# Performance work log

Hardware: AMD Instinct MI355X
Metric: run time of the kernel (lower is better)

The kernel has to match this reference:

```python
import jax, jax.numpy as jnp
import numpy as np

NBITS = 16  # posit word size passed to posit_forward
ES = 1      # posit exponent-field size (standard posit16 uses es=1)


def posit_quant(x, nbits=NBITS, es=ES):
    """Round-trip float -> posit(nbits, es) -> float, vectorized.

    Emulates posit quantization: regime length determines how many fraction
    bits remain, mantissa is rounded to that precision, magnitude clamped to
    [minpos, maxpos]. Straight-through estimator keeps gradients useful.
    """
    absx = jnp.abs(x)
    sign = jnp.sign(x)
    safe = jnp.maximum(absx, 1e-30)
    scale = jnp.floor(jnp.log2(safe))                 # binary exponent
    useed_log2 = float(2 ** es)
    regime = jnp.floor(scale / useed_log2)
    rlen = jnp.where(regime >= 0, regime + 2.0, 1.0 - regime)  # regime bits
    fbits = jnp.clip(nbits - 1 - es - rlen, 0.0, 28.0)          # fraction bits left
    pw = jnp.exp2(fbits)
    m = safe * jnp.exp2(-scale)                       # mantissa in [1, 2)
    mq = 1.0 + jnp.round((m - 1.0) * pw) / pw
    maxscale = float((nbits - 2) * (2 ** es))         # maxpos = 2^((n-2)*2^es)
    mag = jnp.clip(mq * jnp.exp2(scale), jnp.exp2(-maxscale), jnp.exp2(maxscale))
    q = jnp.where(absx == 0.0, 0.0, sign * mag)
    return x + jax.lax.stop_gradient(q - x)           # straight-through


def posit_linear(x, W, b):
    # posit_forward: quantize operands, GEMM, quantize the accumulated output
    xq = posit_quant(x)
    Wq = posit_quant(W)
    bq = posit_quant(b)
    return posit_quant(xq @ Wq.T + bq)


def setup_inputs() -> dict:
    key = jax.random.key(0)
    ks = jax.random.split(key, 7)

    def w(k, o, i):
        return jax.random.normal(k, (o, i), jnp.float32) * (1.0 / np.sqrt(i))

    return {
        "x": jax.random.normal(ks[0], (4096, 2048), jnp.float32),
        "W0": w(ks[1], 8192, 2048),
        "b0": jax.random.normal(ks[2], (8192,), jnp.float32) * 0.01,
        "W1": w(ks[3], 8192, 8192),
        "b1": jax.random.normal(ks[4], (8192,), jnp.float32) * 0.01,
        "W2": w(ks[5], 2048, 8192),
        "b2": jax.random.normal(ks[6], (2048,), jnp.float32) * 0.01,
    }


def reference(x, W0, b0, W1, b1, W2, b2):
    # layer 0: posit linear + relu (clamp(min=0))
    h = jax.nn.relu(posit_linear(x, W0, b0))
    # layer 1: posit linear + relu
    h = jax.nn.relu(posit_linear(h, W1, b1))
    # layer 2: posit linear, identity activation
    return posit_linear(h, W2, b2)
```

## Files before the change

### kernel.cpp

```cpp
#include <hip/hip_runtime.h>
#include <hip/hip_bf16.h>
#include <cstdint>
#include <cstddef>

using bf16 = __hip_bfloat16;
typedef __attribute__((ext_vector_type(8))) short short8;
typedef __attribute__((ext_vector_type(4))) float f32x4;

__device__ __forceinline__ float posit_quant_f32(float x) {
  float absx = fabsf(x);
  float safe = fmaxf(absx, 1e-30f);
  uint32_t bits = __float_as_uint(safe);
  int scale = (int)((bits >> 23) & 0xFFu) - 127;
  int regime = scale >> 1;
  int rlen = (regime >= 0) ? (regime + 2) : (1 - regime);
  int fbits = 14 - rlen;
  fbits = fbits < 0 ? 0 : fbits;
  float pw = (float)(1 << fbits);
  float m = __uint_as_float((bits & 0x007FFFFFu) | 0x3F800000u);
  float mq = rintf((m - 1.0f) * pw) * (1.0f / pw) + 1.0f;
  float mag = mq * __uint_as_float((uint32_t)(scale + 127) << 23);
  mag = fminf(fmaxf(mag, 0x1p-28f), 0x1p28f);
  return (absx == 0.0f) ? 0.0f : copysignf(mag, x);
}

__global__ void kquant_bf16(const float* __restrict__ in, bf16* __restrict__ out, long n4) {
  long i = (long)blockIdx.x * blockDim.x + threadIdx.x;
  long stride = (long)gridDim.x * blockDim.x;
  for (; i < n4; i += stride) {
    float4 v = ((const float4*)in)[i];
    ushort4 o;
    o.x = __builtin_bit_cast(unsigned short, __float2bfloat16(posit_quant_f32(v.x)));
    o.y = __builtin_bit_cast(unsigned short, __float2bfloat16(posit_quant_f32(v.y)));
    o.z = __builtin_bit_cast(unsigned short, __float2bfloat16(posit_quant_f32(v.z)));
    o.w = __builtin_bit_cast(unsigned short, __float2bfloat16(posit_quant_f32(v.w)));
    ((ushort4*)out)[i] = o;
  }
}

__global__ void kquant_f32(const float* __restrict__ in, float* __restrict__ out, int n) {
  int i = blockIdx.x * blockDim.x + threadIdx.x;
  if (i < n) out[i] = posit_quant_f32(in[i]);
}

typedef __attribute__((address_space(1))) uint32_t gu32;
typedef __attribute__((address_space(3))) uint32_t lu32;

#define SBAR()  do { __builtin_amdgcn_sched_barrier(0); __builtin_amdgcn_s_barrier(); \
                     __builtin_amdgcn_sched_barrier(0); } while (0)
#define LGKM0() do { asm volatile("s_waitcnt lgkmcnt(0)" ::: "memory"); \
                     __builtin_amdgcn_sched_barrier(0); } while (0)
#define VMCNT(N) asm volatile("s_waitcnt vmcnt(" #N ")" ::: "memory")

#define STG_A(BUF, H, KT) do { \
    const char* _s = srcA + (long)((H) * 128) * Kb + (long)(KT) * 128; \
    char* _d = smem + (BUF) * 32768 + (H) * 16384 + dA; \
    __builtin_amdgcn_global_load_lds((const gu32*)_s, (lu32*)_d, 16, 0, 0); \
    __builtin_amdgcn_global_load_lds((const gu32*)(_s + 64 * Kb), (lu32*)(_d + 8192), 16, 0, 0); \
  } while (0)
#define STG_B(BUF, H, KT) do { \
    const char* _s = srcB + (long)((H) * 128) * Kb + (long)(KT) * 128; \
    char* _d = smem + (BUF) * 32768 + (H) * 16384 + dB; \
    __builtin_amdgcn_global_load_lds((const gu32*)_s, (lu32*)_d, 16, 0, 0); \
    __builtin_amdgcn_global_load_lds((const gu32*)(_s + 64 * Kb), (lu32*)(_d + 8192), 16, 0, 0); \
  } while (0)

#define LDA8(BUF, FI, CK) (*(const short8*)(smem + (BUF) * 32768 + aBase + (FI) * 2048 + (CK)))
#define LDB8(BUF, FJ, CK) (*(const short8*)(smem + (BUF) * 32768 + bBase + (FJ) * 2048 + (CK)))

#define MQ(FI0, FJ0) do { \
    _Pragma("unroll") \
    for (int fi = 0; fi < 4; ++fi) { \
      _Pragma("unroll") \
      for (int fj = 0; fj < 2; ++fj) { \
        acc[(FI0) + fi][(FJ0) + fj] = __builtin_amdgcn_mfma_f32_16x16x32_bf16( \
            afr[fi][0], bfr[(FJ0) + fj][0], acc[(FI0) + fi][(FJ0) + fj], 0, 0, 0); \
        acc[(FI0) + fi][(FJ0) + fj] = __builtin_amdgcn_mfma_f32_16x16x32_bf16( \
            afr[fi][1], bfr[(FJ0) + fj][1], acc[(FI0) + fi][(FJ0) + fj], 0, 0, 0); \
      } \
    } \
  } while (0)

template <bool RELU, bool OUTBF16>
__global__ __launch_bounds__(512, 2) void gemm256_posit(
    const bf16* __restrict__ A, const bf16* __restrict__ B,
    const float* __restrict__ bias, void* __restrict__ out,
    int M, int N, int K, int nbx, int cpx) {
  __shared__ char smem[131072];

  const int tid  = threadIdx.x;
  const int lane = tid & 63;
  const int wave = tid >> 6;
  const int wr = wave >> 2;
  const int wc = wave & 3;

  const int flat = blockIdx.x;
  const int wgid = (flat & 7) * cpx + (flat >> 3);
  const long brow0 = (long)(wgid / nbx) * 256;
  const long bcol0 = (long)(wgid % nbx) * 256;

  const long Kb = (long)K * 2;
  const int srow = tid >> 3;
  const int scb  = ((tid & 7) * 16) ^ (((tid >> 3) & 7) << 4);
  const char* srcA = (const char*)A + (brow0 + srow) * Kb + scb;
  const char* srcB = (const char*)B + (bcol0 + srow) * Kb + scb;
  const int dA = wave * 1024;
  const int dB = 65536 + wave * 1024;

  const int fr  = lane & 15;
  const int swz = (lane & 7) << 4;
  const int ck0 = (((lane >> 4) << 4)) ^ swz;
  const int ck1 = (64 + ((lane >> 4) << 4)) ^ swz;
  const int aBase = wr * 16384 + fr * 128;
  const int bBase = 65536 + wc * 8192 + fr * 128;

  f32x4 acc[8][4] = {};
  short8 afr[4][2], bfr[4][2];

  const int nkt = K >> 6;
  const int np  = nkt >> 1;

  STG_B(0, 0, 0); STG_B(0, 1, 0);
  STG_A(0, 0, 0); STG_A(0, 1, 0);
  STG_B(1, 0, 1); STG_B(1, 1, 1);
  VMCNT(4);
  SBAR();

#pragma unroll 1
  for (int i = 0; i < np; ++i) {
    const int kA1 = 2 * i + 1;
    const int kS2 = (2 * i + 2) & (nkt - 1);
    const int kS3 = (2 * i + 3) & (nkt - 1);

#pragma unroll
    for (int f = 0; f < 4; ++f) { afr[f][0] = LDA8(0, f, ck0); afr[f][1] = LDA8(0, f, ck1); }
#pragma unroll
    for (int f = 0; f < 2; ++f) { bfr[f][0] = LDB8(0, f, ck0); bfr[f][1] = LDB8(0, f, ck1); }
    STG_A(1, 0, kA1);
    SBAR(); LGKM0();
    __builtin_amdgcn_s_setprio(1); MQ(0, 0); __builtin_amdgcn_s_setprio(0);
    SBAR();

#pragma unroll
    for (int f = 2; f < 4; ++f) { bfr[f][0] = LDB8(0, f, ck0); bfr[f][1] = LDB8(0, f, ck1); }
    STG_A(1, 1, kA1);
    SBAR(); LGKM0();
    __builtin_amdgcn_s_setprio(1); MQ(0, 2); __builtin_amdgcn_s_setprio(0);
    SBAR();

#pragma unroll
    for (int f = 0; f < 4; ++f) { afr[f][0] = LDA8(0, f + 4, ck0); afr[f][1] = LDA8(0, f + 4, ck1); }
    STG_B(0, 0, kS2);
    SBAR(); LGKM0();
    __builtin_amdgcn_s_setprio(1); MQ(4, 0); __builtin_amdgcn_s_setprio(0);
    SBAR();

    STG_B(0, 1, kS2);
    VMCNT(4);
    SBAR();
    __builtin_amdgcn_s_setprio(1); MQ(4, 2); __builtin_amdgcn_s_setprio(0);
    SBAR();

#pragma unroll
    for (int f = 0; f < 4; ++f) { afr[f][0] = LDA8(1, f, ck0); afr[f][1] = LDA8(1, f, ck1); }
#pragma unroll
    for (int f = 0; f < 2; ++f) { bfr[f][0] = LDB8(1, f, ck0); bfr[f][1] = LDB8(1, f, ck1); }
    STG_A(0, 0, kS2);
    SBAR(); LGKM0();
    __builtin_amdgcn_s_setprio(1); MQ(0, 0); __builtin_amdgcn_s_setprio(0);
    SBAR();

#pragma unroll
    for (int f = 2; f < 4; ++f) { bfr[f][0] = LDB8(1, f, ck0); bfr[f][1] = LDB8(1, f, ck1); }
    STG_A(0, 1, kS2);
    SBAR(); LGKM0();
    __builtin_amdgcn_s_setprio(1); MQ(0, 2); __builtin_amdgcn_s_setprio(0);
    SBAR();

#pragma unroll
    for (int f = 0; f < 4; ++f) { afr[f][0] = LDA8(1, f + 4, ck0); afr[f][1] = LDA8(1, f + 4, ck1); }
    STG_B(1, 0, kS3);
    SBAR(); LGKM0();
    __builtin_amdgcn_s_setprio(1); MQ(4, 0); __builtin_amdgcn_s_setprio(0);
    SBAR();

    STG_B(1, 1, kS3);
    VMCNT(4);
    SBAR();
    __builtin_amdgcn_s_setprio(1); MQ(4, 2); __builtin_amdgcn_s_setprio(0);
    SBAR();
  }
  asm volatile("s_waitcnt vmcnt(0)" ::: "memory");

  const int orow = (lane >> 4) * 4;
  const long row0 = brow0 + wr * 128;
  const long col0 = bcol0 + wc * 64;
#pragma unroll
  for (int fj = 0; fj < 4; ++fj) {
    const long col = col0 + fj * 16 + fr;
    const float bv = bias[col];
#pragma unroll
    for (int fi = 0; fi < 8; ++fi) {
#pragma unroll
      for (int q = 0; q < 4; ++q) {
        float v = acc[fi][fj][q] + bv;
        v = posit_quant_f32(v);
        if (RELU) v = fmaxf(v, 0.0f);
        const long idx = (row0 + fi * 16 + orow + q) * (long)N + col;
        if (OUTBF16) ((bf16*)out)[idx] = __float2bfloat16(v);
        else         ((float*)out)[idx] = v;
      }
    }
  }
}

#define GBM 128
#define GBN 128
#define GBK 32

__device__ __forceinline__ void gload_lds16(const void* g, void* l) {
  __builtin_amdgcn_global_load_lds((const gu32*)g, (lu32*)l, 16, 0, 0);
}

template <bool RELU, bool OUTBF16>
__global__ __launch_bounds__(256, 2) void gemm_bt_posit(
    const bf16* __restrict__ A, const bf16* __restrict__ B,
    const float* __restrict__ bias, void* __restrict__ out,
    int M, int N, int K) {
  __shared__ __align__(1024) bf16 sA[GBM][GBK];
  __shared__ __align__(1024) bf16 sB[GBN][GBK];

  const int tid = threadIdx.x;
  const int lane = tid & 63;
  const int wave = tid >> 6;
  const int wr = wave >> 1;
  const int wc = wave & 1;
  const long brow0 = (long)blockIdx.y * GBM;
  const long bcol0 = (long)blockIdx.x * GBN;

  const int srow = lane >> 2;
  const int scol = (lane & 3) * 8;
  const int seg0 = wave * 2;

  const bf16* gA0 = A + (brow0 + seg0 * 16 + srow) * (long)K + scol;
  const bf16* gA1 = A + (brow0 + seg0 * 16 + 16 + srow) * (long)K + scol;
  const bf16* gB0 = B + (bcol0 + seg0 * 16 + srow) * (long)K + scol;
  const bf16* gB1 = B + (bcol0 + seg0 * 16 + 16 + srow) * (long)K + scol;
  bf16* lA0 = (bf16*)sA + seg0 * 512;
  bf16* lA1 = lA0 + 512;
  bf16* lB0 = (bf16*)sB + seg0 * 512;
  bf16* lB1 = lB0 + 512;

  f32x4 acc[4][4] = {};
  const int fr = lane & 15;
  const int fk = (lane >> 4) * 8;

  for (int kt = 0; kt < K; kt += GBK) {
    __syncthreads();
    gload_lds16(gA0 + kt, lA0);
    gload_lds16(gA1 + kt, lA1);
    gload_lds16(gB0 + kt, lB0);
    gload_lds16(gB1 + kt, lB1);
    __syncthreads();

    short8 af[4], bfv[4];
#pragma unroll
    for (int i = 0; i < 4; ++i) af[i] = *(const short8*)&sA[wr * 64 + i * 16 + fr][fk];
#pragma unroll
    for (int j = 0; j < 4; ++j) bfv[j] = *(const short8*)&sB[wc * 64 + j * 16 + fr][fk];
#pragma unroll
    for (int i = 0; i < 4; ++i)
#pragma unroll
      for (int j = 0; j < 4; ++j)
        acc[i][j] = __builtin_amdgcn_mfma_f32_16x16x32_bf16(af[i], bfv[j], acc[i][j], 0, 0, 0);
  }

  const int orow = (lane >> 4) * 4;
  const long row0 = brow0 + wr * 64;
  const long col0 = bcol0 + wc * 64;
#pragma unroll
  for (int j = 0; j < 4; ++j) {
    const long col = col0 + j * 16 + fr;
    const float bv = bias[col];
#pragma unroll
    for (int i = 0; i < 4; ++i) {
#pragma unroll
      for (int q = 0; q < 4; ++q) {
        float v = acc[i][j][q] + bv;
        v = posit_quant_f32(v);
        if (RELU) v = fmaxf(v, 0.0f);
        const long idx = (row0 + i * 16 + orow + q) * (long)N + col;
        if (OUTBF16) ((bf16*)out)[idx] = __float2bfloat16(v);
        else         ((float*)out)[idx] = v;
      }
    }
  }
}

extern "C" void kernel_launch(void* const* d_in, const int* in_sizes, int n_in,
                              void* d_out, int out_size, void* d_ws, size_t ws_size,
                              hipStream_t stream) {
  const float* x  = (const float*)d_in[0];
  const float* W0 = (const float*)d_in[1];
  const float* b0 = (const float*)d_in[2];
  const float* W1 = (const float*)d_in[3];
  const float* b1 = (const float*)d_in[4];
  const float* W2 = (const float*)d_in[5];
  const float* b2 = (const float*)d_in[6];

  const int M = 4096, D0 = 2048, D1 = 8192, D2 = 8192, DO = 2048;

  char* ws = (char*)d_ws;
  size_t off = 0;
  auto alloc = [&](size_t bytes) {
    char* p = ws + off;
    off += (bytes + 255) & ~(size_t)255;
    return p;
  };
  bf16* xq  = (bf16*)alloc((size_t)M * D0 * 2);
  bf16* W0q = (bf16*)alloc((size_t)D1 * D0 * 2);
  bf16* W1q = (bf16*)alloc((size_t)D2 * D1 * 2);
  bf16* W2q = (bf16*)alloc((size_t)DO * D2 * 2);
  bf16* h0  = (bf16*)alloc((size_t)M * D1 * 2);
  bf16* h1  = (bf16*)alloc((size_t)M * D2 * 2);
  float* b0q = (float*)alloc((size_t)D1 * 4);
  float* b1q = (float*)alloc((size_t)D2 * 4);
  float* b2q = (float*)alloc((size_t)DO * 4);
  (void)ws_size; (void)in_sizes; (void)n_in; (void)out_size;

  auto quant = [&](const float* in, bf16* outp, long n) {
    long n4 = n / 4;
    long want = (n4 + 255) / 256;
    int blocks = (int)(want < 2048 ? want : 2048);
    kquant_bf16<<<blocks, 256, 0, stream>>>(in, outp, n4);
  };
  quant(x,  xq,  (long)M * D0);
  quant(W0, W0q, (long)D1 * D0);
  quant(W1, W1q, (long)D2 * D1);
  quant(W2, W2q, (long)DO * D2);
  kquant_f32<<<(D1 + 255) / 256, 256, 0, stream>>>(b0, b0q, D1);
  kquant_f32<<<(D2 + 255) / 256, 256, 0, stream>>>(b1, b1q, D2);
  kquant_f32<<<(DO + 255) / 256, 256, 0, stream>>>(b2, b2q, DO);

  {
    int nbx = D1 / 256, nwg = nbx * (M / 256);
    gemm256_posit<true, true><<<dim3(nwg), dim3(512), 0, stream>>>(
        xq, W0q, b0q, h0, M, D1, D0, nbx, nwg / 8);
  }
  {
    int nbx = D2 / 256, nwg = nbx * (M / 256);
    gemm256_posit<true, true><<<dim3(nwg), dim3(512), 0, stream>>>(
        h0, W1q, b1q, h1, M, D2, D1, nbx, nwg / 8);
  }
  gemm_bt_posit<false, false><<<dim3(DO / GBN, M / GBM), dim3(256), 0, stream>>>(
      h1, W2q, b2q, (float*)d_out, M, DO, D2);
}
```

Measured before the change: 941.1 us.

## Split-K the last GEMM onto the 256 kernel, triple-buffer A, fold bias quant

The final 4096x2048x8192 layer now runs on the large 256x256 tile kernel with split-K=2, which gives 256 workgroups instead of 128. Each split writes fp32 partials, and a new combine kernel adds them, applies the posit-quantized bias and quantizes the output. The GEMM's LDS grows to 160KB so A can be triple-buffered with a rotating buffer index, and the three bias quant kernels are dropped by quantizing the bias inline in the epilogue. In exchange the last layer writes and reads an extra 64MB of partials, and the larger LDS may lower occupancy for the first two GEMMs.

```diff
diff --git a/kernel.cpp b/kernel.cpp
--- a/kernel.cpp
+++ b/kernel.cpp
@@ -38,9 +38,21 @@
   }
 }
 
-__global__ void kquant_f32(const float* __restrict__ in, float* __restrict__ out, int n) {
-  int i = blockIdx.x * blockDim.x + threadIdx.x;
-  if (i < n) out[i] = posit_quant_f32(in[i]);
+__global__ void kcombine(const float* __restrict__ p, const float* __restrict__ bias,
+                         float* __restrict__ out, long n4, long halfn, int cmask) {
+  long i = (long)blockIdx.x * blockDim.x + threadIdx.x;
+  long stride = (long)gridDim.x * blockDim.x;
+  for (; i < n4; i += stride) {
+    float4 a = ((const float4*)p)[i];
+    float4 b = ((const float4*)(p + halfn))[i];
+    int c0 = (int)(i & cmask) * 4;
+    float4 o;
+    o.x = posit_quant_f32(a.x + b.x + posit_quant_f32(bias[c0 + 0]));
+    o.y = posit_quant_f32(a.y + b.y + posit_quant_f32(bias[c0 + 1]));
+    o.z = posit_quant_f32(a.z + b.z + posit_quant_f32(bias[c0 + 2]));
+    o.w = posit_quant_f32(a.w + b.w + posit_quant_f32(bias[c0 + 3]));
+    ((float4*)out)[i] = o;
+  }
 }
 
 typedef __attribute__((address_space(1))) uint32_t gu32;
@@ -52,21 +64,18 @@
                      __builtin_amdgcn_sched_barrier(0); } while (0)
 #define VMCNT(N) asm volatile("s_waitcnt vmcnt(" #N ")" ::: "memory")
 
-#define STG_A(BUF, H, KT) do { \
-    const char* _s = srcA + (long)((H) * 128) * Kb + (long)(KT) * 128; \
-    char* _d = smem + (BUF) * 32768 + (H) * 16384 + dA; \
+#define STG(SRC, KT, H, DST) do { \
+    const char* _s = (SRC) + (long)((H) * 128) * Kb + (long)(KT) * 128; \
+    char* _d = smem + (DST) + (H) * 16384 + wave * 1024; \
     __builtin_amdgcn_global_load_lds((const gu32*)_s, (lu32*)_d, 16, 0, 0); \
     __builtin_amdgcn_global_load_lds((const gu32*)(_s + 64 * Kb), (lu32*)(_d + 8192), 16, 0, 0); \
   } while (0)
-#define STG_B(BUF, H, KT) do { \
-    const char* _s = srcB + (long)((H) * 128) * Kb + (long)(KT) * 128; \
-    char* _d = smem + (BUF) * 32768 + (H) * 16384 + dB; \
-    __builtin_amdgcn_global_load_lds((const gu32*)_s, (lu32*)_d, 16, 0, 0); \
-    __builtin_amdgcn_global_load_lds((const gu32*)(_s + 64 * Kb), (lu32*)(_d + 8192), 16, 0, 0); \
-  } while (0)
-
-#define LDA8(BUF, FI, CK) (*(const short8*)(smem + (BUF) * 32768 + aBase + (FI) * 2048 + (CK)))
-#define LDB8(BUF, FJ, CK) (*(const short8*)(smem + (BUF) * 32768 + bBase + (FJ) * 2048 + (CK)))
+
+#define LDA8(AOFF, FI, CK) (*(const short8*)(smem + (AOFF) + aRel + (FI) * 2048 + (CK)))
+#define LDB8(BOFF, FJ, CK) (*(const short8*)(smem + (BOFF) + bRel + (FJ) * 2048 + (CK)))
+
+#define BB0 98304
+#define BB1 131072
 
 #define MQ(FI0, FJ0) do { \
     _Pragma("unroll") \
@@ -81,12 +90,12 @@
     } \
   } while (0)
 
-template <bool RELU, bool OUTBF16>
+template <int MODE>
 __global__ __launch_bounds__(512, 2) void gemm256_posit(
     const bf16* __restrict__ A, const bf16* __restrict__ B,
     const float* __restrict__ bias, void* __restrict__ out,
-    int M, int N, int K, int nbx, int cpx) {
-  __shared__ char smem[131072];
+    int M, int N, int Kfull, int Kloop, int nbt, int cpx) {
+  __shared__ __align__(1024) char smem[163840];
 
   const int tid  = threadIdx.x;
   const int lane = tid & 63;
@@ -96,119 +105,129 @@
 
   const int flat = blockIdx.x;
   const int wgid = (flat & 7) * cpx + (flat >> 3);
-  const long brow0 = (long)(wgid / nbx) * 256;
-  const long bcol0 = (long)(wgid % nbx) * 256;
-
-  const long Kb = (long)K * 2;
+  const int split = wgid / nbt;
+  const int t = wgid - split * nbt;
+  const int nbx = N >> 8;
+  const long brow0 = (long)(t / nbx) * 256;
+  const long bcol0 = (long)(t % nbx) * 256;
+
+  const long Kb = (long)Kfull * 2;
+  const long splitoff = (long)split * Kloop * 2;
+
   const int srow = tid >> 3;
   const int scb  = ((tid & 7) * 16) ^ (((tid >> 3) & 7) << 4);
-  const char* srcA = (const char*)A + (brow0 + srow) * Kb + scb;
-  const char* srcB = (const char*)B + (bcol0 + srow) * Kb + scb;
-  const int dA = wave * 1024;
-  const int dB = 65536 + wave * 1024;
+  const char* srcA = (const char*)A + (brow0 + srow) * Kb + scb + splitoff;
+  const char* srcB = (const char*)B + (bcol0 + srow) * Kb + scb + splitoff;
 
   const int fr  = lane & 15;
   const int swz = (lane & 7) << 4;
   const int ck0 = (((lane >> 4) << 4)) ^ swz;
   const int ck1 = (64 + ((lane >> 4) << 4)) ^ swz;
-  const int aBase = wr * 16384 + fr * 128;
-  const int bBase = 65536 + wc * 8192 + fr * 128;
+  const int aRel = wr * 16384 + fr * 128;
+  const int bRel = wc * 8192 + fr * 128;
 
   f32x4 acc[8][4] = {};
   short8 afr[4][2], bfr[4][2];
 
-  const int nkt = K >> 6;
+  const int nkt = Kloop >> 6;
   const int np  = nkt >> 1;
 
-  STG_B(0, 0, 0); STG_B(0, 1, 0);
-  STG_A(0, 0, 0); STG_A(0, 1, 0);
-  STG_B(1, 0, 1); STG_B(1, 1, 1);
-  VMCNT(4);
+  int a0 = 0, a1 = 32768, a2 = 65536;
+
+  STG(srcA, 0, 0, 0);     STG(srcA, 0, 1, 0);
+  STG(srcB, 0, 0, BB0);   STG(srcB, 0, 1, BB0);
+  STG(srcA, 1, 0, 32768); STG(srcA, 1, 1, 32768);
+  STG(srcB, 1, 0, BB1);   STG(srcB, 1, 1, BB1);
+  VMCNT(8);
   SBAR();
 
 #pragma unroll 1
   for (int i = 0; i < np; ++i) {
-    const int kA1 = 2 * i + 1;
     const int kS2 = (2 * i + 2) & (nkt - 1);
     const int kS3 = (2 * i + 3) & (nkt - 1);
 
 #pragma unroll
-    for (int f = 0; f < 4; ++f) { afr[f][0] = LDA8(0, f, ck0); afr[f][1] = LDA8(0, f, ck1); }
-#pragma unroll
-    for (int f = 0; f < 2; ++f) { bfr[f][0] = LDB8(0, f, ck0); bfr[f][1] = LDB8(0, f, ck1); }
-    STG_A(1, 0, kA1);
+    for (int f = 0; f < 4; ++f) { afr[f][0] = LDA8(a0, f, ck0); afr[f][1] = LDA8(a0, f, ck1); }
+#pragma unroll
+    for (int f = 0; f < 2; ++f) { bfr[f][0] = LDB8(BB0, f, ck0); bfr[f][1] = LDB8(BB0, f, ck1); }
+    STG(srcA, kS2, 0, a2);
     SBAR(); LGKM0();
     __builtin_amdgcn_s_setprio(1); MQ(0, 0); __builtin_amdgcn_s_setprio(0);
     SBAR();
 
 #pragma unroll
-    for (int f = 2; f < 4; ++f) { bfr[f][0] = LDB8(0, f, ck0); bfr[f][1] = LDB8(0, f, ck1); }
-    STG_A(1, 1, kA1);
+    for (int f = 2; f < 4; ++f) { bfr[f][0] = LDB8(BB0, f, ck0); bfr[f][1] = LDB8(BB0, f, ck1); }
+    STG(srcA, kS2, 1, a2);
     SBAR(); LGKM0();
     __builtin_amdgcn_s_setprio(1); MQ(0, 2); __builtin_amdgcn_s_setprio(0);
     SBAR();
 
 #pragma unroll
-    for (int f = 0; f < 4; ++f) { afr[f][0] = LDA8(0, f + 4, ck0); afr[f][1] = LDA8(0, f + 4, ck1); }
-    STG_B(0, 0, kS2);
+    for (int f = 0; f < 4; ++f) { afr[f][0] = LDA8(a0, f + 4, ck0); afr[f][1] = LDA8(a0, f + 4, ck1); }
+    STG(srcB, kS2, 0, BB0);
     SBAR(); LGKM0();
     __builtin_amdgcn_s_setprio(1); MQ(4, 0); __builtin_amdgcn_s_setprio(0);
     SBAR();
 
-    STG_B(0, 1, kS2);
-    VMCNT(4);
+    STG(srcB, kS2, 1, BB0);
+    VMCNT(8);
     SBAR();
     __builtin_amdgcn_s_setprio(1); MQ(4, 2); __builtin_amdgcn_s_setprio(0);
     SBAR();
 
 #pragma unroll
-    for (int f = 0; f < 4; ++f) { afr[f][0] = LDA8(1, f, ck0); afr[f][1] = LDA8(1, f, ck1); }
-#pragma unroll
-    for (int f = 0; f < 2; ++f) { bfr[f][0] = LDB8(1, f, ck0); bfr[f][1] = LDB8(1, f, ck1); }
-    STG_A(0, 0, kS2);
+    for (int f = 0; f < 4; ++f) { afr[f][0] = LDA8(a1, f, ck0); afr[f][1] = LDA8(a1, f, ck1); }
+#pragma unroll
+    for (int f = 0; f < 2; ++f) { bfr[f][0] = LDB8(BB1, f, ck0); bfr[f][1] = LDB8(BB1, f, ck1); }
+    STG(srcA, kS3, 0, a0);
     SBAR(); LGKM0();
     __builtin_amdgcn_s_setprio(1); MQ(0, 0); __builtin_amdgcn_s_setprio(0);
     SBAR();
 
 #pragma unroll
-    for (int f = 2; f < 4; ++f) { bfr[f][0] = LDB8(1, f, ck0); bfr[f][1] = LDB8(1, f, ck1); }
-    STG_A(0, 1, kS2);
+    for (int f = 2; f < 4; ++f) { bfr[f][0] = LDB8(BB1, f, ck0); bfr[f][1] = LDB8(BB1, f, ck1); }
+    STG(srcA, kS3, 1, a0);
     SBAR(); LGKM0();
     __builtin_amdgcn_s_setprio(1); MQ(0, 2); __builtin_amdgcn_s_setprio(0);
     SBAR();
 
 #pragma unroll
-    for (int f = 0; f < 4; ++f) { afr[f][0] = LDA8(1, f + 4, ck0); afr[f][1] = LDA8(1, f + 4, ck1); }
-    STG_B(1, 0, kS3);
+    for (int f = 0; f < 4; ++f) { afr[f][0] = LDA8(a1, f + 4, ck0); afr[f][1] = LDA8(a1, f + 4, ck1); }
+    STG(srcB, kS3, 0, BB1);
     SBAR(); LGKM0();
     __builtin_amdgcn_s_setprio(1); MQ(4, 0); __builtin_amdgcn_s_setprio(0);
     SBAR();
 
-    STG_B(1, 1, kS3);
-    VMCNT(4);
+    STG(srcB, kS3, 1, BB1);
+    VMCNT(8);
     SBAR();
     __builtin_amdgcn_s_setprio(1); MQ(4, 2); __builtin_amdgcn_s_setprio(0);
     SBAR();
+
+    int tmp = a2; a2 = a1; a1 = a0; a0 = tmp;
   }
   asm volatile("s_waitcnt vmcnt(0)" ::: "memory");
 
   const int orow = (lane >> 4) * 4;
   const long row0 = brow0 + wr * 128;
   const long col0 = bcol0 + wc * 64;
+  const long obase = (MODE == 2) ? (long)split * M * N : 0;
 #pragma unroll
   for (int fj = 0; fj < 4; ++fj) {
     const long col = col0 + fj * 16 + fr;
-    const float bv = bias[col];
+    const float bv = (MODE == 2) ? 0.0f : posit_quant_f32(bias[col]);
 #pragma unroll
     for (int fi = 0; fi < 8; ++fi) {
 #pragma unroll
       for (int q = 0; q < 4; ++q) {
-        float v = acc[fi][fj][q] + bv;
-        v = posit_quant_f32(v);
-        if (RELU) v = fmaxf(v, 0.0f);
-        const long idx = (row0 + fi * 16 + orow + q) * (long)N + col;
-        if (OUTBF16) ((bf16*)out)[idx] = __float2bfloat16(v);
-        else         ((float*)out)[idx] = v;
+        float v = acc[fi][fj][q];
+        if (MODE != 2) {
+          v = posit_quant_f32(v + bv);
+          if (MODE == 0) v = fmaxf(v, 0.0f);
+        }
+        const long idx = obase + (row0 + fi * 16 + orow + q) * (long)N + col;
+        if (MODE == 0) ((bf16*)out)[idx] = __float2bfloat16(v);
+        else           ((float*)out)[idx] = v;
       }
     }
   }
@@ -281,13 +300,12 @@
 #pragma unroll
   for (int j = 0; j < 4; ++j) {
     const long col = col0 + j * 16 + fr;
-    const float bv = bias[col];
+    const float bv = posit_quant_f32(bias[col]);
 #pragma unroll
     for (int i = 0; i < 4; ++i) {
 #pragma unroll
       for (int q = 0; q < 4; ++q) {
-        float v = acc[i][j][q] + bv;
-        v = posit_quant_f32(v);
+        float v = posit_quant_f32(acc[i][j][q] + bv);
         if (RELU) v = fmaxf(v, 0.0f);
         const long idx = (row0 + i * 16 + orow + q) * (long)N + col;
         if (OUTBF16) ((bf16*)out)[idx] = __float2bfloat16(v);
@@ -323,10 +341,9 @@
   bf16* W2q = (bf16*)alloc((size_t)DO * D2 * 2);
   bf16* h0  = (bf16*)alloc((size_t)M * D1 * 2);
   bf16* h1  = (bf16*)alloc((size_t)M * D2 * 2);
-  float* b0q = (float*)alloc((size_t)D1 * 4);
-  float* b1q = (float*)alloc((size_t)D2 * 4);
-  float* b2q = (float*)alloc((size_t)DO * 4);
-  (void)ws_size; (void)in_sizes; (void)n_in; (void)out_size;
+  float* part = (float*)alloc((size_t)2 * M * DO * 4);
+  const bool splitk = (off <= ws_size);
+  (void)in_sizes; (void)n_in; (void)out_size;
 
   auto quant = [&](const float* in, bf16* outp, long n) {
     long n4 = n / 4;
@@ -338,20 +355,27 @@
   quant(W0, W0q, (long)D1 * D0);
   quant(W1, W1q, (long)D2 * D1);
   quant(W2, W2q, (long)DO * D2);
-  kquant_f32<<<(D1 + 255) / 256, 256, 0, stream>>>(b0, b0q, D1);
-  kquant_f32<<<(D2 + 255) / 256, 256, 0, stream>>>(b1, b1q, D2);
-  kquant_f32<<<(DO + 255) / 256, 256, 0, stream>>>(b2, b2q, DO);
 
   {
-    int nbx = D1 / 256, nwg = nbx * (M / 256);
-    gemm256_posit<true, true><<<dim3(nwg), dim3(512), 0, stream>>>(
-        xq, W0q, b0q, h0, M, D1, D0, nbx, nwg / 8);
+    int nbt = (D1 / 256) * (M / 256), nwg = nbt;
+    gemm256_posit<0><<<dim3(nwg), dim3(512), 0, stream>>>(
+        xq, W0q, b0, h0, M, D1, D0, D0, nbt, nwg / 8);
   }
   {
-    int nbx = D2 / 256, nwg = nbx * (M / 256);
-    gemm256_posit<true, true><<<dim3(nwg), dim3(512), 0, stream>>>(
-        h0, W1q, b1q, h1, M, D2, D1, nbx, nwg / 8);
-  }
-  gemm_bt_posit<false, false><<<dim3(DO / GBN, M / GBM), dim3(256), 0, stream>>>(
-      h1, W2q, b2q, (float*)d_out, M, DO, D2);
-}
+    int nbt = (D2 / 256) * (M / 256), nwg = nbt;
+    gemm256_posit<0><<<dim3(nwg), dim3(512), 0, stream>>>(
+        h0, W1q, b1, h1, M, D2, D1, D1, nbt, nwg / 8);
+  }
+  if (splitk) {
+    int nbt = (DO / 256) * (M / 256);
+    int nwg = nbt * 2;
+    gemm256_posit<2><<<dim3(nwg), dim3(512), 0, stream>>>(
+        h1, W2q, nullptr, part, M, DO, D2, D2 / 2, nbt, nwg / 8);
+    long n4 = (long)M * DO / 4;
+    kcombine<<<2048, 256, 0, stream>>>(part, b2, (float*)d_out, n4,
+                                       (long)M * DO, DO / 4 - 1);
+  } else {
+    gemm_bt_posit<false, false><<<dim3(DO / GBN, M / GBM), dim3(256), 0, stream>>>(
+        h1, W2q, b2, (float*)d_out, M, DO, D2);
+  }
+}
```

New measurement: 894.6 us. 4.9% less time.
